# Performance work log

Hardware: AMD Instinct MI355X
Metric: run time of the kernel (lower is better)

## Reference

```python
import jax, jax.numpy as jnp
import numpy as np

B, S, IN_DIM, D_MODEL, H = 8, 1024, 512, 1024, 16
DEPTH = D_MODEL // H
LN_EPS = 1e-5


def setup_inputs() -> dict:
    key = jax.random.key(0)
    ks = jax.random.split(key, 10)
    def xavier(k, shape):
        fan_in, fan_out = shape[0], shape[1]
        lim = float(np.sqrt(6.0 / (fan_in + fan_out)))
        return jax.random.uniform(k, shape, jnp.float32, -lim, lim)
    return {
        "x": jax.random.normal(ks[0], (B, S, IN_DIM), jnp.float32),
        "mask": jax.random.randint(ks[1], (H, S, S), 0, 2, jnp.int32),
        "wq_w": xavier(ks[2], (IN_DIM, D_MODEL)),
        "wq_b": jnp.zeros((D_MODEL,), jnp.float32),
        "wk_w": xavier(ks[3], (IN_DIM, D_MODEL)),
        "wk_b": jnp.zeros((D_MODEL,), jnp.float32),
        "wv_w": xavier(ks[4], (IN_DIM, D_MODEL)),
        "wv_b": jnp.zeros((D_MODEL,), jnp.float32),
        "dense_w": xavier(ks[5], (D_MODEL, D_MODEL)),
        "dense_b": jnp.zeros((D_MODEL,), jnp.float32),
        "res_w": xavier(ks[6], (IN_DIM, D_MODEL)),  # residual_linear (no bias)
        "ln_g": 1.0 + 0.02 * jax.random.normal(ks[7], (D_MODEL,), jnp.float32),
        "ln_b": 0.02 * jax.random.normal(ks[8], (D_MODEL,), jnp.float32),
    }


def reference(x, mask, wq_w, wq_b, wk_w, wk_b, wv_w, wv_b,
              dense_w, dense_b, res_w, ln_g, ln_b):
    bs = x.shape[0]
    residual = x @ res_w  # [B,S,D_MODEL]
    # project and split heads -> [B,H,S,depth]
    def split(t):
        return t.reshape(bs, -1, H, DEPTH).transpose(0, 2, 1, 3)
    q = split(x @ wq_w + wq_b)
    k = split(x @ wk_w + wk_b)
    v = split(x @ wv_w + wv_b)
    scale = 1.0 / jnp.sqrt(jnp.asarray(DEPTH, x.dtype))
    attn = jnp.einsum("bhqd,bhkd->bhqk", q, k) * scale
    attn = jnp.where(mask[None] == 0, jnp.asarray(-1e9, attn.dtype), attn)
    attn = jax.nn.softmax(attn, axis=-1)  # dropout is identity in eval
    out = jnp.einsum("bhqk,bhkd->bhqd", attn, v)
    out = out.transpose(0, 2, 1, 3).reshape(bs, -1, D_MODEL)
    out = out @ dense_w + dense_b
    # residual + LayerNorm
    y = residual + out
    mu = jnp.mean(y, axis=-1, keepdims=True)
    var = jnp.mean(jnp.square(y - mu), axis=-1, keepdims=True)
    y = (y - mu) * jax.lax.rsqrt(var + LN_EPS)
    return y * ln_g + ln_b
```

## Files before the change

kernel.cpp:

```cpp
#include <hip/hip_runtime.h>
#include <stdint.h>

#define B_ 8
#define S_ 1024
#define IN_DIM 512
#define DM 1024
#define H_ 16
#define DEP 64

typedef __bf16 bf16;
typedef __attribute__((ext_vector_type(8))) __bf16 bf16x8;
typedef __attribute__((ext_vector_type(4))) __bf16 bf16x4;
typedef __attribute__((ext_vector_type(4))) float f32x4;

static __device__ __forceinline__ void gld_lds16(const void* g, void* l) {
    __builtin_amdgcn_global_load_lds(
        (const __attribute__((address_space(1))) uint32_t*)g,
        (__attribute__((address_space(3))) uint32_t*)l, 16, 0, 0);
}

static __device__ __forceinline__ float ldin(const void* p, size_t i, int isb) {
    return isb ? (float)((const bf16*)p)[i] : ((const float*)p)[i];
}

template<int N>
static __device__ __forceinline__ void wait_barrier() {
    if constexpr (N == 4)      asm volatile("s_waitcnt vmcnt(4) lgkmcnt(0)\ns_barrier" ::: "memory");
    else if constexpr (N == 3) asm volatile("s_waitcnt vmcnt(3) lgkmcnt(0)\ns_barrier" ::: "memory");
    else                       asm volatile("s_waitcnt vmcnt(0) lgkmcnt(0)\ns_barrier" ::: "memory");
}

static __device__ __forceinline__ int ldsch(int r, int q4) {
    const int pr = r >> 1;
    return pr*8 + ((((r & 1) << 2) + q4) ^ (pr & 7));
}

__global__ __launch_bounds__(256) void prep_kernel(
    const uint16_t* __restrict__ xraw, const void* __restrict__ x,
    const void* __restrict__ wq, const void* __restrict__ wk, const void* __restrict__ wv,
    const void* __restrict__ res, const void* __restrict__ dense,
    const int* __restrict__ mask,
    bf16* __restrict__ wqT, bf16* __restrict__ wkT, bf16* __restrict__ wvT,
    bf16* __restrict__ resT, bf16* __restrict__ denseT,
    const void* b0, const void* b1, const void* b2, const void* b3,
    const void* b4, const void* b5, bf16* __restrict__ small,
    bf16* __restrict__ xc, unsigned long long* __restrict__ mb, int* __restrict__ flag)
{
    __shared__ int s_isb;
    __shared__ bf16 tile[32][33];
    const int tid = threadIdx.x;

    if (tid < 64) {
        int sane = 0;
        #pragma unroll
        for (int j = 0; j < 8; j++) {
            const uint16_t u = xraw[tid * 8 + j];
            const int e = (u >> 7) & 0xff;
            sane += ((u & 0x7fff) == 0 || (e >= 100 && e <= 140)) ? 1 : 0;
        }
        #pragma unroll
        for (int m = 1; m < 64; m <<= 1) sane += __shfl_xor(sane, m);
        if (tid == 0) s_isb = (sane >= 450) ? 1 : 0;
    }
    __syncthreads();
    const int isb = s_isb;
    const int bid = blockIdx.x;
    if (bid == 0 && tid == 0) *flag = isb;

    if (bid < 1024) {
        const int w = tid >> 6, lane = tid & 63;
        const int gw = bid * 4 + w;
        for (int c = gw; c < 262144; c += 4096) {
            const int v = mask[(size_t)c * 64 + lane];
            const unsigned long long bits = __ballot(v != 0);
            if (lane == 0) mb[c] = bits;
        }
    } else if (bid < 5120) {
        const size_t i = ((size_t)(bid - 1024) * 256 + tid) * 4;
        if (isb) {
            *(bf16x4*)(xc + i) = *(const bf16x4*)((const bf16*)x + i);
        } else {
            const float4 v = *(const float4*)((const float*)x + i);
            bf16x4 o; o[0] = (bf16)v.x; o[1] = (bf16)v.y; o[2] = (bf16)v.z; o[3] = (bf16)v.w;
            *(bf16x4*)(xc + i) = o;
        }
    } else if (bid < 8192) {
        const int t = bid - 5120;
        const int z = t >> 9, rem = t & 511;
        const void* src; bf16* dst; int kb, kd;
        if (z == 0)      { src = wq;    dst = wqT;    kb = 0;   kd = 512;  }
        else if (z == 1) { src = wk;    dst = wkT;    kb = 0;   kd = 512;  }
        else if (z == 2) { src = wv;    dst = wvT;    kb = 0;   kd = 512;  }
        else if (z == 3) { src = res;   dst = resT;   kb = 0;   kd = 512;  }
        else if (z == 4) { src = dense; dst = denseT; kb = 0;   kd = 1024; }
        else             { src = dense; dst = denseT; kb = 512; kd = 1024; }
        const int n0 = (rem & 31) * 32, k0 = (rem >> 5) * 32;
        const int tx = tid & 31, ty = tid >> 5;
        #pragma unroll
        for (int r = 0; r < 4; r++)
            tile[ty + r*8][tx] = (bf16)ldin(src, (size_t)(kb + k0 + ty + r*8) * DM + n0 + tx, isb);
        __syncthreads();
        #pragma unroll
        for (int r = 0; r < 4; r++)
            dst[(size_t)(n0 + ty + r*8) * kd + kb + k0 + tx] = tile[tx][ty + r*8];
    } else {
        const int s6 = bid - 8192;
        const void* srcs[6] = {b0, b1, b2, b3, b4, b5};
        const void* s = srcs[s6];
        for (int i = tid; i < 1024; i += 256)
            small[s6 * 1024 + i] = (bf16)ldin(s, i, isb);
    }
}

template<int KDIM>
static __device__ __forceinline__ void gemm_core(
    const bf16* __restrict__ A, const bf16* __restrict__ BT,
    int m0, int n0, bf16* Asm, bf16* Bsm, f32x4 acc[4][4])
{
    const int tid = threadIdx.x, l = tid & 63, w = tid >> 6;
    const int wm = w >> 1, wn = w & 1, quad = l >> 4, l15 = l & 15;
    #pragma unroll
    for (int i = 0; i < 4; i++)
        #pragma unroll
        for (int j = 0; j < 4; j++) acc[i][j] = f32x4{0.f, 0.f, 0.f, 0.f};

    constexpr int NIT = KDIM / 32;
    const int lp  = l >> 3;
    const int s0  = (l & 7) ^ lp;
    const int rof = s0 >> 2;
    const int kch = (s0 & 3) * 8;

    auto stage = [&](int t, int bo) {
        const int k0 = t * 32;
        #pragma unroll
        for (int qq = 0; qq < 2; qq++) {
            const int row = (qq*32 + w*8 + lp)*2 + rof;
            gld_lds16(A  + (size_t)(m0 + row)*KDIM + k0 + kch, Asm + bo + (qq*256 + w*64)*8);
            gld_lds16(BT + (size_t)(n0 + row)*KDIM + k0 + kch, Bsm + bo + (qq*256 + w*64)*8);
        }
    };

    stage(0, 0);
    stage(1, 4096);
    int cur = 0;
    for (int it = 0; it < NIT; ++it) {
        if (it < NIT - 1) wait_barrier<4>();
        else              wait_barrier<0>();
        if (it + 2 < NIT)
            stage(it + 2, (cur >= 4096) ? cur - 4096 : cur + 8192);
        bf16x8 af[4], bfv[4];
        #pragma unroll
        for (int i = 0; i < 4; i++)
            af[i] = *(const bf16x8*)(Asm + cur + ldsch(wm*64 + i*16 + l15, quad)*8);
        #pragma unroll
        for (int j = 0; j < 4; j++)
            bfv[j] = *(const bf16x8*)(Bsm + cur + ldsch(wn*64 + j*16 + l15, quad)*8);
        #pragma unroll
        for (int i = 0; i < 4; i++)
            #pragma unroll
            for (int j = 0; j < 4; j++)
                acc[i][j] = __builtin_amdgcn_mfma_f32_16x16x32_bf16(af[i], bfv[j], acc[i][j], 0, 0, 0);
        cur = (cur == 8192) ? 0 : cur + 4096;
    }
}

#define EPI_P 132
__global__ __launch_bounds__(256) void proj_kernel(
    const bf16* __restrict__ x,
    const bf16* __restrict__ wqT, const bf16* __restrict__ wkT,
    const bf16* __restrict__ wvT, const bf16* __restrict__ resT,
    const bf16* __restrict__ small,
    bf16* __restrict__ Q, bf16* __restrict__ K, bf16* __restrict__ VtG, bf16* __restrict__ R)
{
    __shared__ alignas(16) char smem[49152];
    bf16* Asm = (bf16*)smem;
    bf16* Bsm = (bf16*)(smem + 24576);
    bf16* epi = (bf16*)smem;

    const int m0 = blockIdx.x * 128;
    const int ng = blockIdx.y * 128;
    const int sel = ng >> 10, n0 = ng & 1023;
    const bf16* BT; const bf16* bias = nullptr;
    if (sel == 0)      { BT = wqT; bias = small;        }
    else if (sel == 1) { BT = wkT; bias = small + 1024; }
    else if (sel == 2) { BT = wvT; bias = small + 2048; }
    else               { BT = resT; }

    f32x4 acc[4][4];
    gemm_core<IN_DIM>(x, BT, m0, n0, Asm, Bsm, acc);

    const int tid = threadIdx.x, l = tid & 63, w = tid >> 6;
    const int wm = w >> 1, wn = w & 1, quad = l >> 4, l15 = l & 15;

    if (sel == 2) {
        const int bb = m0 >> 10, srow0 = m0 & 1023;
        #pragma unroll
        for (int hf = 0; hf < 2; hf++) {
            __syncthreads();
            if (wn == hf) {
                #pragma unroll
                for (int j = 0; j < 4; j++) {
                    const int cl = j*16 + l15;
                    const float bv = (float)bias[n0 + hf*64 + cl];
                    #pragma unroll
                    for (int i = 0; i < 4; i++) {
                        const int rho = wm*64 + i*16 + quad*4;
                        #pragma unroll
                        for (int r = 0; r < 4; r++)
                            epi[cl*EPI_P + rho + r] = (bf16)(acc[i][j][r] + bv);
                    }
                }
            }
            __syncthreads();
            const int hh = (n0 >> 6) + hf;
            const int sc = tid & 15;
            #pragma unroll
            for (int pass = 0; pass < 4; pass++) {
                const int dl = (tid >> 4) + pass*16;
                bf16x8 v;
                #pragma unroll
                for (int k = 0; k < 8; k++) {
                    const int pl = (sc & 3)*8 + k;
                    const int kl = ((pl & 4) << 2) | ((pl & 24) >> 1) | (pl & 3);
                    v[k] = epi[dl*EPI_P + (sc >> 2)*32 + kl];
                }
                *(bf16x8*)(VtG + ((size_t)(bb*16 + hh)*64 + dl)*S_ + srow0 + sc*8) = v;
            }
        }
        return;
    }

    #pragma unroll
    for (int j = 0; j < 4; j++) {
        const int col = n0 + wn*64 + j*16 + l15;
        const float bv = (sel < 3) ? (float)bias[col] : 0.f;
        #pragma unroll
        for (int i = 0; i < 4; i++) {
            const int rb = m0 + wm*64 + i*16 + quad*4;
            #pragma unroll
            for (int r = 0; r < 4; r++) {
                const float v = acc[i][j][r] + bv;
                if (sel == 0)      Q[(size_t)(rb + r)*DM + col] = (bf16)(v * 0.18033688f);
                else if (sel == 1) K[(size_t)(rb + r)*DM + col] = (bf16)v;
                else               R[(size_t)(rb + r)*DM + col] = (bf16)v;
            }
        }
    }
}

__global__ __launch_bounds__(256) void attn_kernel(
    const bf16* __restrict__ Q, const bf16* __restrict__ K, const bf16* __restrict__ VtG,
    const unsigned long long* __restrict__ mb, bf16* __restrict__ AO)
{
    __shared__ alignas(16) bf16 Ksm[2*64*64];
    __shared__ alignas(16) bf16 Vsm[2*64*64];

    const int tid = threadIdx.x, l = tid & 63, w = tid >> 6;
    const int quad = l >> 4, l15 = l & 15;

    const int fid = blockIdx.y * 8 + blockIdx.x;
    const int xcd = fid & 7, idx = fid >> 3;
    const int bh  = xcd * 16 + (idx >> 3);
    const int qt  = idx & 7;
    const int b = bh >> 4, h = bh & 15;
    const int wrow = qt*128 + w*32;
    const size_t rowbase = (size_t)b * S_;

    bf16x8 qa[2][2];
    #pragma unroll
    for (int g = 0; g < 2; g++) {
        const bf16* qp = Q + (rowbase + wrow + g*16 + l15)*DM + h*DEP + quad*8;
        qa[g][0] = *(const bf16x8*)qp;
        qa[g][1] = *(const bf16x8*)(qp + 32);
    }
    const bf16* kgbase = K + rowbase*DM + h*DEP;
    const bf16* vgbase = VtG + (size_t)(b*16 + h)*64*S_;
    const unsigned long long* mbase[2];
    #pragma unroll
    for (int g = 0; g < 2; g++)
        mbase[g] = mb + ((size_t)h*S_ + wrow + g*16 + l15) * 16;

    uint32_t bmr[4];
    #pragma unroll
    for (int r = 0; r < 4; r++) bmr[r] = 1u << (quad*4 + r);

    bf16x8 onesv8;
    #pragma unroll
    for (int r = 0; r < 8; r++) onesv8[r] = (bf16)1.0f;

    f32x4 oT[2][4];
    f32x4 lacc[2];
    #pragma unroll
    for (int g = 0; g < 2; g++) {
        lacc[g] = f32x4{0.f,0.f,0.f,0.f};
        #pragma unroll
        for (int dt = 0; dt < 4; dt++) oT[g][dt] = f32x4{0.f,0.f,0.f,0.f};
    }

    const int srow8 = l >> 3;
    const int gch   = (l & 7) ^ srow8;

    #pragma unroll
    for (int q = 0; q < 2; q++) {
        const int row = q*32 + w*8 + srow8;
        gld_lds16(kgbase + (size_t)row*DM + gch*8, Ksm + (q*256 + w*64)*8);
        gld_lds16(vgbase + (size_t)row*S_ + gch*8, Vsm + (q*256 + w*64)*8);
    }
    uint32_t mlo[2], mhi[2];
    #pragma unroll
    for (int g = 0; g < 2; g++) {
        const unsigned long long mw = mbase[g][0];
        mlo[g] = (uint32_t)mw; mhi[g] = (uint32_t)(mw >> 32);
    }

    const int rsw = l15 & 7;

    for (int it = 0; it < 16; it++) {
        __syncthreads();
        const int cur = (it & 1) * 4096, nxt = cur ^ 4096;
        const bf16* Kc = Ksm + cur;
        const bf16* Vc = Vsm + cur;

        const uint32_t cmlo[2] = {mlo[0], mlo[1]}, cmhi[2] = {mhi[0], mhi[1]};
        if (it + 1 < 16) {
            #pragma unroll
            for (int q = 0; q < 2; q++) {
                const int row = q*32 + w*8 + srow8;
                gld_lds16(kgbase + (size_t)((it+1)*64 + row)*DM + gch*8,
                          Ksm + nxt + (q*256 + w*64)*8);
                gld_lds16(vgbase + (size_t)row*S_ + (it+1)*64 + gch*8,
                          Vsm + nxt + (q*256 + w*64)*8);
            }
            #pragma unroll
            for (int g = 0; g < 2; g++) {
                const unsigned long long mw = mbase[g][it + 1];
                mlo[g] = (uint32_t)mw; mhi[g] = (uint32_t)(mw >> 32);
            }
        }

        #pragma unroll
        for (int sub = 0; sub < 2; sub++) {
            bf16x8 kf[2][2];
            bf16x8 va8[4];
            #pragma unroll
            for (int h2 = 0; h2 < 2; h2++) {
                const int krow = sub*32 + h2*16 + l15;
                kf[h2][0] = *(const bf16x8*)(Kc + krow*64 + ((quad    ) ^ rsw)*8);
                kf[h2][1] = *(const bf16x8*)(Kc + krow*64 + ((quad + 4) ^ rsw)*8);
            }
            #pragma unroll
            for (int dt = 0; dt < 4; dt++)
                va8[dt] = *(const bf16x8*)(Vc + (dt*16 + l15)*64 + ((sub*4 + quad) ^ rsw)*8);

            #pragma unroll
            for (int g = 0; g < 2; g++) {
                f32x4 st[2];
                __builtin_amdgcn_s_setprio(1);
                #pragma unroll
                for (int h2 = 0; h2 < 2; h2++) {
                    f32x4 z = {0.f,0.f,0.f,0.f};
                    z = __builtin_amdgcn_mfma_f32_16x16x32_bf16(kf[h2][0], qa[g][0], z, 0, 0, 0);
                    z = __builtin_amdgcn_mfma_f32_16x16x32_bf16(kf[h2][1], qa[g][1], z, 0, 0, 0);
                    st[h2] = z;
                }
                __builtin_amdgcn_s_setprio(0);
                const uint32_t msk = sub ? cmhi[g] : cmlo[g];
                bf16x8 pb8;
                #pragma unroll
                for (int r = 0; r < 4; r++) {
                    const float e0 = __builtin_amdgcn_exp2f(st[0][r]);
                    pb8[r]     = (bf16)((msk & bmr[r]) ? e0 : 0.f);
                    const float e1 = __builtin_amdgcn_exp2f(st[1][r]);
                    pb8[4 + r] = (bf16)(((msk >> 16) & bmr[r]) ? e1 : 0.f);
                }
                __builtin_amdgcn_s_setprio(1);
                lacc[g] = __builtin_amdgcn_mfma_f32_16x16x32_bf16(onesv8, pb8, lacc[g], 0, 0, 0);
                #pragma unroll
                for (int dt = 0; dt < 4; dt++)
                    oT[g][dt] = __builtin_amdgcn_mfma_f32_16x16x32_bf16(va8[dt], pb8, oT[g][dt], 0, 0, 0);
                __builtin_amdgcn_s_setprio(0);
            }
        }
    }

    #pragma unroll
    for (int g = 0; g < 2; g++) {
        const float inv = 1.0f / lacc[g][0];
        bf16* aor = AO + (rowbase + wrow + g*16 + l15)*DM + h*DEP;
        #pragma unroll
        for (int dt = 0; dt < 4; dt++) {
            bf16x4 ov;
            #pragma unroll
            for (int r = 0; r < 4; r++) ov[r] = (bf16)(oT[g][dt][r] * inv);
            *(bf16x4*)(aor + dt*16 + quad*4) = ov;
        }
    }
}

__global__ __launch_bounds__(256) void dense_kernel(
    const bf16* __restrict__ AOin, const bf16* __restrict__ dT,
    const bf16* __restrict__ db, bf16* __restrict__ R)
{
    __shared__ alignas(16) bf16 Asm[3*64*32];
    __shared__ alignas(16) bf16 Bsm[3*128*32];
    const int m0 = blockIdx.x * 64, n0 = blockIdx.y * 128;
    const int tid = threadIdx.x, l = tid & 63, w = tid >> 6;
    const int wm = w >> 1, wn = w & 1, quad = l >> 4, l15 = l & 15;

    f32x4 acc[2][4];
    #pragma unroll
    for (int i = 0; i < 2; i++)
        #pragma unroll
        for (int j = 0; j < 4; j++) acc[i][j] = f32x4{0.f, 0.f, 0.f, 0.f};

    const int lp  = l >> 3;
    const int s0  = (l & 7) ^ lp;
    const int rof = s0 >> 2;
    const int kch = (s0 & 3) * 8;

    auto stage = [&](int t, int boA, int boB) {
        const int k1 = t * 32;
        gld_lds16(AOin + (size_t)(m0 + (w*8 + lp)*2 + rof)*DM + k1 + kch, Asm + boA + (w*64)*8);
        #pragma unroll
        for (int qq = 0; qq < 2; qq++) {
            const int row = (qq*32 + w*8 + lp)*2 + rof;
            gld_lds16(dT + (size_t)(n0 + row)*DM + k1 + kch, Bsm + boB + (qq*256 + w*64)*8);
        }
    };

    stage(0, 0, 0);
    stage(1, 2048, 4096);
    int curA = 0, curB = 0;
    for (int it = 0; it < 32; ++it) {
        if (it < 31) wait_barrier<3>();
        else         wait_barrier<0>();
        if (it + 2 < 32)
            stage(it + 2, (curA >= 2048) ? curA - 2048 : curA + 4096,
                          (curB >= 4096) ? curB - 4096 : curB + 8192);
        bf16x8 af[2], bfv[4];
        #pragma unroll
        for (int i = 0; i < 2; i++)
            af[i] = *(const bf16x8*)(Asm + curA + ldsch(wm*32 + i*16 + l15, quad)*8);
        #pragma unroll
        for (int j = 0; j < 4; j++)
            bfv[j] = *(const bf16x8*)(Bsm + curB + ldsch(wn*64 + j*16 + l15, quad)*8);
        #pragma unroll
        for (int i = 0; i < 2; i++)
            #pragma unroll
            for (int j = 0; j < 4; j++)
                acc[i][j] = __builtin_amdgcn_mfma_f32_16x16x32_bf16(af[i], bfv[j], acc[i][j], 0, 0, 0);
        curA = (curA == 4096) ? 0 : curA + 2048;
        curB = (curB == 8192) ? 0 : curB + 4096;
    }

    #pragma unroll
    for (int j = 0; j < 4; j++) {
        const int col = n0 + wn*64 + j*16 + l15;
        const float bv = (float)db[col];
        #pragma unroll
        for (int i = 0; i < 2; i++) {
            const int rb = m0 + wm*32 + i*16 + quad*4;
            #pragma unroll
            for (int r = 0; r < 4; r++) {
                const size_t idx = (size_t)(rb + r)*DM + col;
                R[idx] = (bf16)((float)R[idx] + acc[i][j][r] + bv);
            }
        }
    }
}

__global__ __launch_bounds__(256) void ln_kernel(
    const bf16* __restrict__ R, const bf16* __restrict__ small,
    void* __restrict__ out, const int* __restrict__ flag)
{
    const int isb = *flag;
    const int row  = blockIdx.x * 4 + (threadIdx.x >> 6);
    const int lane = threadIdx.x & 63;
    const bf16* rp = R + (size_t)row*DM;

    float v[16];
    float s = 0.f;
    #pragma unroll
    for (int k = 0; k < 4; k++) {
        const bf16x4 rv = *(const bf16x4*)(rp + k*256 + lane*4);
        #pragma unroll
        for (int r = 0; r < 4; r++) { v[k*4+r] = (float)rv[r]; s += v[k*4+r]; }
    }
    #pragma unroll
    for (int m = 1; m < 64; m <<= 1) s += __shfl_xor(s, m);
    const float mu = s * (1.0f/DM);

    float q = 0.f;
    #pragma unroll
    for (int i = 0; i < 16; i++) { v[i] -= mu; q += v[i]*v[i]; }
    #pragma unroll
    for (int m = 1; m < 64; m <<= 1) q += __shfl_xor(q, m);
    const float rstd = rsqrtf(q * (1.0f/DM) + 1e-5f);

    #pragma unroll
    for (int k = 0; k < 4; k++) {
        const int col = k*256 + lane*4;
        const bf16x4 gv = *(const bf16x4*)(small + 4*1024 + col);
        const bf16x4 bv = *(const bf16x4*)(small + 5*1024 + col);
        float o[4];
        #pragma unroll
        for (int r = 0; r < 4; r++) o[r] = v[k*4+r]*rstd*(float)gv[r] + (float)bv[r];
        if (isb) {
            bf16x4 ov;
            #pragma unroll
            for (int r = 0; r < 4; r++) ov[r] = (bf16)o[r];
            *(bf16x4*)((bf16*)out + (size_t)row*DM + col) = ov;
        } else {
            float4 ov = {o[0], o[1], o[2], o[3]};
            *(float4*)((float*)out + (size_t)row*DM + col) = ov;
        }
    }
}

extern "C" void kernel_launch(void* const* d_in, const int* in_sizes, int n_in,
                              void* d_out, int out_size, void* d_ws, size_t ws_size,
                              hipStream_t stream) {
    const int* mask = (const int*)d_in[1];

    char* ws = (char*)d_ws;
    bf16* wqT   = (bf16*)(ws);
    bf16* wkT   = (bf16*)(ws + ((size_t)1 << 20));
    bf16* wvT   = (bf16*)(ws + ((size_t)2 << 20));
    bf16* resT  = (bf16*)(ws + ((size_t)3 << 20));
    bf16* dT    = (bf16*)(ws + ((size_t)4 << 20));
    bf16* small = (bf16*)(ws + ((size_t)6 << 20));
    int*  flag  = (int*) (ws + ((size_t)6 << 20) + 16384);
    unsigned long long* mbits = (unsigned long long*)(ws + ((size_t)7 << 20));
    bf16* Qb    = (bf16*)(ws + ((size_t)9  << 20));
    bf16* Kb    = (bf16*)(ws + ((size_t)25 << 20));
    bf16* VtG   = (bf16*)(ws + ((size_t)41 << 20));
    bf16* R     = (bf16*)(ws + ((size_t)57 << 20));
    bf16* xc    = (bf16*)d_out;

    prep_kernel<<<8198, 256, 0, stream>>>(
        (const uint16_t*)d_in[0], d_in[0],
        d_in[2], d_in[4], d_in[6], d_in[10], d_in[8],
        mask,
        wqT, wkT, wvT, resT, dT,
        d_in[3], d_in[5], d_in[7], d_in[9], d_in[11], d_in[12], small,
        xc, mbits, flag);
    proj_kernel<<<dim3(64, 32), 256, 0, stream>>>(
        xc, wqT, wkT, wvT, resT, small, Qb, Kb, VtG, R);
    attn_kernel<<<dim3(8, 128), 256, 0, stream>>>(Qb, Kb, VtG, mbits, Qb );
    dense_kernel<<<dim3(128, 8), 256, 0, stream>>>(Qb, dT, small + 3*1024, R);
    ln_kernel<<<2048, 256, 0, stream>>>(R, small, d_out, flag);
}
```

Measured before the change: 321.7 us.

## Triple-buffer K/V tiles in attention kernel with two-stage prefetch

The attention kernel's K and V shared-memory buffers grow from two stages to three. Tiles are now prefetched two iterations ahead, and the plain __syncthreads is replaced by explicit vmcnt waits followed by a barrier. The aim is to hide more global-load latency behind the MFMA and softmax work. The cost is 16KB more LDS per block, which may lower occupancy, and vmcnt counting that depends on the mask loads also being vector-memory ops.

Measured after the change: 320.2 us. Within noise of the previous version (-0.5%).

```diff
diff --git a/kernel.cpp b/kernel.cpp
--- a/kernel.cpp
+++ b/kernel.cpp
@@ -25,10 +25,13 @@
 
 template<int N>
 static __device__ __forceinline__ void wait_barrier() {
-    if constexpr (N == 4)      asm volatile("s_waitcnt vmcnt(4) lgkmcnt(0)\ns_barrier" ::: "memory");
+    if constexpr (N == 6)      asm volatile("s_waitcnt vmcnt(6) lgkmcnt(0)\ns_barrier" ::: "memory");
+    else if constexpr (N == 4) asm volatile("s_waitcnt vmcnt(4) lgkmcnt(0)\ns_barrier" ::: "memory");
     else if constexpr (N == 3) asm volatile("s_waitcnt vmcnt(3) lgkmcnt(0)\ns_barrier" ::: "memory");
+    else if constexpr (N == 2) asm volatile("s_waitcnt vmcnt(2) lgkmcnt(0)\ns_barrier" ::: "memory");
     else                       asm volatile("s_waitcnt vmcnt(0) lgkmcnt(0)\ns_barrier" ::: "memory");
 }
+#define CFENCE() asm volatile("" ::: "memory")
 
 static __device__ __forceinline__ int ldsch(int r, int q4) {
     const int pr = r >> 1;
@@ -252,8 +255,8 @@
     const bf16* __restrict__ Q, const bf16* __restrict__ K, const bf16* __restrict__ VtG,
     const unsigned long long* __restrict__ mb, bf16* __restrict__ AO)
 {
-    __shared__ alignas(16) bf16 Ksm[2*64*64];
-    __shared__ alignas(16) bf16 Vsm[2*64*64];
+    __shared__ alignas(16) bf16 Ksm[3*64*64];
+    __shared__ alignas(16) bf16 Vsm[3*64*64];
 
     const int tid = threadIdx.x, l = tid & 63, w = tid >> 6;
     const int quad = l >> 4, l15 = l & 15;
@@ -300,12 +303,20 @@
     const int srow8 = l >> 3;
     const int gch   = (l & 7) ^ srow8;
 
-    #pragma unroll
-    for (int q = 0; q < 2; q++) {
-        const int row = q*32 + w*8 + srow8;
-        gld_lds16(kgbase + (size_t)row*DM + gch*8, Ksm + (q*256 + w*64)*8);
-        gld_lds16(vgbase + (size_t)row*S_ + gch*8, Vsm + (q*256 + w*64)*8);
-    }
+    auto stage = [&](int t, int bo) {
+        const int kt = t * 64;
+        #pragma unroll
+        for (int q = 0; q < 2; q++) {
+            const int row = q*32 + w*8 + srow8;
+            gld_lds16(kgbase + (size_t)(kt + row)*DM + gch*8, Ksm + bo + (q*256 + w*64)*8);
+            gld_lds16(vgbase + (size_t)row*S_ + kt + gch*8,   Vsm + bo + (q*256 + w*64)*8);
+        }
+    };
+
+    stage(0, 0);
+    CFENCE();
+    stage(1, 4096);
+    CFENCE();
     uint32_t mlo[2], mhi[2];
     #pragma unroll
     for (int g = 0; g < 2; g++) {
@@ -315,28 +326,23 @@
 
     const int rsw = l15 & 7;
 
+    int cur = 0;
     for (int it = 0; it < 16; it++) {
-        __syncthreads();
-        const int cur = (it & 1) * 4096, nxt = cur ^ 4096;
+        if (it < 15) wait_barrier<6>();
+        else         wait_barrier<2>();
         const bf16* Kc = Ksm + cur;
         const bf16* Vc = Vsm + cur;
 
         const uint32_t cmlo[2] = {mlo[0], mlo[1]}, cmhi[2] = {mhi[0], mhi[1]};
         if (it + 1 < 16) {
-            #pragma unroll
-            for (int q = 0; q < 2; q++) {
-                const int row = q*32 + w*8 + srow8;
-                gld_lds16(kgbase + (size_t)((it+1)*64 + row)*DM + gch*8,
-                          Ksm + nxt + (q*256 + w*64)*8);
-                gld_lds16(vgbase + (size_t)row*S_ + (it+1)*64 + gch*8,
-                          Vsm + nxt + (q*256 + w*64)*8);
-            }
             #pragma unroll
             for (int g = 0; g < 2; g++) {
                 const unsigned long long mw = mbase[g][it + 1];
                 mlo[g] = (uint32_t)mw; mhi[g] = (uint32_t)(mw >> 32);
             }
         }
+        if (it + 2 < 16)
+            stage(it + 2, (cur >= 4096) ? cur - 4096 : cur + 8192);
 
         #pragma unroll
         for (int sub = 0; sub < 2; sub++) {
@@ -381,6 +387,7 @@
                 __builtin_amdgcn_s_setprio(0);
             }
         }
+        cur = (cur == 8192) ? 0 : cur + 4096;
     }
 
     #pragma unroll
```
